# Kernel optimization log

Hardware: AMD Instinct MI355X
Metric: run time of the kernel (lower is better)

The kernel has to match this reference:

```python
import jax, jax.numpy as jnp
import numpy as np

N = 100000   # nodes
E = 600000   # edges
F = 128      # node_feat
HID = 128    # hidden
H = 4        # heads
D = HID // H # head dim
NT = 3       # node types
ET = 4       # edge types
SLOPE = 0.2  # leaky relu slope for attention logits


def hetero_linear(x, types, W, b):
    # per-type linear: out[n] = x[n] @ W[types[n]] + b[types[n]]
    # one-hot contraction avoids gathering a full [N,in,out] weight tensor
    T = W.shape[0]
    oh = jax.nn.one_hot(types, T, dtype=x.dtype)
    return jnp.einsum('ni,nt,tio->no', x, oh, W) + b[types]


def setup_inputs() -> dict:
    key = jax.random.key(0)
    ks = jax.random.split(key, 20)
    f32 = jnp.float32
    s_in = 1.0 / np.sqrt(F)
    s_h = 1.0 / np.sqrt(HID)
    inp = {
        'x': jax.random.normal(ks[0], (N, F), f32),
        'edge_index': jax.random.randint(ks[1], (2, E), 0, N),
        'node_type': jax.random.randint(ks[2], (N,), 0, NT),
        'edge_type': jax.random.randint(ks[3], (E,), 0, ET),
        'edge_attr': jax.random.normal(ks[4], (E, 1), f32),
        # EHATConv params: per-node-type q/k/v projections
        'Wq': jax.random.normal(ks[5], (NT, F, HID), f32) * s_in,
        'Wk': jax.random.normal(ks[6], (NT, F, HID), f32) * s_in,
        'Wv': jax.random.normal(ks[7], (NT, F, HID), f32) * s_in,
        # per-head attention vectors
        'att_src': jax.random.normal(ks[8], (H, D), f32) * s_h,
        'att_dst': jax.random.normal(ks[9], (H, D), f32) * s_h,
        'att_edge': jax.random.normal(ks[10], (H, D), f32) * s_h,
        # per-edge-type edge-attr embedding (edge_dim=1 -> hidden)
        'We': jax.random.normal(ks[11], (ET, 1, HID), f32),
        'be': jax.random.normal(ks[12], (ET, HID), f32) * s_h,
        # HeteroLinear classifiers
        'Wn': jax.random.normal(ks[13], (NT, HID, 1), f32) * s_h,
        'bn': jnp.zeros((NT, 1), f32),
        'Wec': jax.random.normal(ks[14], (ET, HID, 1), f32) * s_h,
        'bec': jnp.zeros((ET, 1), f32),
    }
    return inp


def reference(x, edge_index, node_type, edge_type, edge_attr,
              Wq, Wk, Wv, att_src, att_dst, att_edge, We, be, Wn, bn, Wec, bec):
    src, dst = edge_index[0], edge_index[1]
    n = x.shape[0]
    e = edge_type.shape[0]

    # forward passes zeros as edge_attr into the conv (as in original module)
    eattr = jnp.zeros((e, 1), x.dtype)

    # per-node-type q/k/v projections -> [N,H,D]
    q = hetero_linear(x, node_type, Wq, jnp.zeros((NT, HID), x.dtype)).reshape(n, H, D)
    k = hetero_linear(x, node_type, Wk, jnp.zeros((NT, HID), x.dtype)).reshape(n, H, D)
    v = hetero_linear(x, node_type, Wv, jnp.zeros((NT, HID), x.dtype)).reshape(n, H, D)

    # per-edge-type edge-attr embedding -> [E,H,D]
    e_emb = (jnp.einsum('ni,nio->no', eattr, We[edge_type]) + be[edge_type]).reshape(e, H, D)

    # attention logits per edge/head
    logits = (jnp.einsum('ehd,hd->eh', k[src], att_src)
              + jnp.einsum('ehd,hd->eh', q[dst], att_dst)
              + jnp.einsum('ehd,hd->eh', e_emb, att_edge))
    logits = jnp.where(logits >= 0, logits, SLOPE * logits)

    # segment softmax over incoming edges of each destination node
    m = jax.ops.segment_max(logits, dst, num_segments=n)  # [N,H]
    p = jnp.exp(logits - m[dst])
    denom = jax.ops.segment_sum(p, dst, num_segments=n)   # [N,H]
    alpha = p / (denom[dst] + 1e-16)                       # [E,H]

    # messages and aggregation
    msg = (v[src] + e_emb) * alpha[:, :, None]             # [E,H,D]
    e_out = msg.reshape(e, HID)
    x_out = jax.ops.segment_sum(e_out, dst, num_segments=n)  # [N,HID]

    # nonlin (relu; dropout identity in eval)
    x_h = jax.nn.relu(x_out)
    e_h = jax.nn.relu(e_out)

    # hetero classifiers
    x_cls = hetero_linear(x_h, node_type, Wn, bn)   # [N,1]
    e_cls = hetero_linear(e_h, edge_type, Wec, bec) # [E,1]
    return (x_cls, e_cls)
```

## Files before the change

kernel.cpp:

```cpp
#include <hip/hip_runtime.h>
#include <hip/hip_bf16.h>


#define NN 100000
#define NE 600000
#define FD 128
#define HIDD 128
#define NH 4
#define DH 32
#define NT 3
#define NET 4
#define SLOPE 0.2f
#define CAP 32
#define NBLK_EDGE 2344
#define NBLK_PRE  33

typedef short bf16x8 __attribute__((ext_vector_type(8)));
typedef float f32x4 __attribute__((ext_vector_type(4)));

#define OFF_V       0UL
#define OFF_KS      25600000UL
#define OFF_QD      27200000UL
#define OFF_R       28800000UL
#define OFF_COUNTS  35200000UL
#define OFF_EDGES   35600128UL
#define OFF_ETL     61200128UL
#define OFF_WPACK   61200256UL
#define OFF_BEP     61396864UL
#define OFF_WECP    61398912UL
#define OFF_WNP     61400960UL
#define OFF_WKQP    61402496UL

__device__ __forceinline__ unsigned int pack_bf16(float a, float b) {
    __hip_bfloat16 ha = __float2bfloat16(a);
    __hip_bfloat16 hb = __float2bfloat16(b);
    unsigned short ua = *reinterpret_cast<unsigned short*>(&ha);
    unsigned short ub = *reinterpret_cast<unsigned short*>(&hb);
    return (unsigned int)ua | ((unsigned int)ub << 16);
}

union U8 { uint4 u; bf16x8 v; };

__global__ void k_build(const int* __restrict__ ei, const int* __restrict__ etype,
                        int* __restrict__ counts, uint2* __restrict__ edges,
                        const float* __restrict__ Wq, const float* __restrict__ Wk,
                        const float* __restrict__ Wv,
                        const float* __restrict__ att_src, const float* __restrict__ att_dst,
                        const float* __restrict__ be, const float* __restrict__ att_edge,
                        const float* __restrict__ Wec, const float* __restrict__ Wn,
                        float* __restrict__ etl, unsigned int* __restrict__ wpack,
                        float* __restrict__ bep, float* __restrict__ wecp,
                        float* __restrict__ wnp, unsigned int* __restrict__ wkqp) {
    if (blockIdx.x >= NBLK_EDGE) {
        int pgid = (blockIdx.x - NBLK_EDGE) * 256 + threadIdx.x;
        if (pgid < 16) {
            int t = pgid >> 2, h = pgid & 3;
            float s = 0.f;
            for (int d = 0; d < DH; ++d) s += be[t * HIDD + h * DH + d] * att_edge[h * DH + d];
            etl[t * NH + h] = s;
        } else if (pgid >= 64 && pgid < 64 + NT * 8 * 4 * 64) {
            int q = pgid - 64;
            int t = q >> 11;
            int rem = q & 2047;
            int ot = rem >> 8;
            int rem2 = rem & 255;
            int kc = rem2 >> 6;
            int l = rem2 & 63;
            int o = ot * 16 + (l & 15);
            int kb = kc * 32 + (l >> 4) * 8;
            unsigned int w[4];
#pragma unroll
            for (int jj = 0; jj < 4; ++jj) {
                float v0 = Wv[((size_t)t * FD + kb + 2 * jj) * HIDD + o];
                float v1 = Wv[((size_t)t * FD + kb + 2 * jj + 1) * HIDD + o];
                w[jj] = pack_bf16(v0, v1);
            }
            uint4 o4 = {w[0], w[1], w[2], w[3]};
            *reinterpret_cast<uint4*>(wpack + (size_t)q * 4) = o4;
        } else if (pgid >= 6208 && pgid < 7616) {
            int p = pgid - 6208;
            int dp = p & 127;
            int col = dp >> 3, ot = dp & 7;
            int od = ot * 16 + col;
            if (p < 512) {
                int t2 = p >> 7;
                bep[p] = be[t2 * HIDD + od];
            } else if (p < 1024) {
                int t2 = (p - 512) >> 7;
                wecp[p - 512] = Wec[t2 * HIDD + od];
            } else {
                int t = (p - 1024) >> 7;
                wnp[p - 1024] = Wn[t * HIDD + od];
            }
        } else if (pgid >= 7616 && pgid < 7616 + NT * 4 * 64) {
            int q2 = pgid - 7616;
            int t = q2 >> 8;
            int rem = q2 & 255;
            int kc = rem >> 6;
            int l = rem & 63;
            int col = l & 15, kg = l >> 4;
            unsigned int w[4];
#pragma unroll
            for (int jj = 0; jj < 4; ++jj) {
                float v01[2];
#pragma unroll
                for (int sub = 0; sub < 2; ++sub) {
                    int k = kc * 32 + kg * 8 + 2 * jj + sub;
                    float s = 0.f;
                    if (col < 4) {
                        const float* wrow = Wk + ((size_t)t * FD + k) * HIDD + col * DH;
                        const float* arow = att_src + col * DH;
                        for (int d = 0; d < DH; ++d) s += wrow[d] * arow[d];
                    } else if (col < 8) {
                        int h = col - 4;
                        const float* wrow = Wq + ((size_t)t * FD + k) * HIDD + h * DH;
                        const float* arow = att_dst + h * DH;
                        for (int d = 0; d < DH; ++d) s += wrow[d] * arow[d];
                    }
                    v01[sub] = s;
                }
                w[jj] = pack_bf16(v01[0], v01[1]);
            }
            uint4 o4 = {w[0], w[1], w[2], w[3]};
            *reinterpret_cast<uint4*>(wkqp + (size_t)q2 * 4) = o4;
        }
        return;
    }
    int i = blockIdx.x * blockDim.x + threadIdx.x;
    if (i < NE) {
        int dst = ei[NE + i];
        int pos = atomicAdd(&counts[dst], 1);
        if (pos < CAP) {
            uint2 rec;
            rec.x = ((unsigned)ei[i] << 2) | (unsigned)etype[i];
            rec.y = (unsigned)i;
            edges[(size_t)dst * CAP + pos] = rec;
        }
    }
}

__global__ __launch_bounds__(256) void k_node(const float* __restrict__ x,
                                              const unsigned short* __restrict__ wpack,
                                              const unsigned short* __restrict__ wkqp,
                                              const int* __restrict__ ntype,
                                              unsigned short* __restrict__ vb, float* __restrict__ ks4,
                                              float* __restrict__ qd4) {
    int wave = threadIdx.x >> 6, lane = threadIdx.x & 63;
    int base = blockIdx.x * 64 + wave * 16;
    if (base >= NN) return;
    int col = lane & 15, kg = lane >> 4;
    int n = base + col;
    int tcol = (n < NN) ? ntype[n] : -1;
    int an = n < NN ? n : NN - 1;

    const float* xp = x + (size_t)an * FD;
    bf16x8 afrag[4];
#pragma unroll
    for (int kc = 0; kc < 4; ++kc) {
        float4 a4 = *reinterpret_cast<const float4*>(xp + kc * 32 + kg * 8);
        float4 b4 = *reinterpret_cast<const float4*>(xp + kc * 32 + kg * 8 + 4);
        U8 u;
        u.u.x = pack_bf16(a4.x, a4.y);
        u.u.y = pack_bf16(a4.z, a4.w);
        u.u.z = pack_bf16(b4.x, b4.y);
        u.u.w = pack_bf16(b4.z, b4.w);
        afrag[kc] = u.v;
    }

    f32x4 acc[8];
#pragma unroll
    for (int ot = 0; ot < 8; ++ot) { f32x4 z = {0.f, 0.f, 0.f, 0.f}; acc[ot] = z; }
    f32x4 akq = {0.f, 0.f, 0.f, 0.f};

    for (int t = 0; t < NT; ++t) {
        if (__ballot(tcol == t) == 0ull) continue;
        bf16x8 am[4];
#pragma unroll
        for (int kc = 0; kc < 4; ++kc) {
            U8 z; z.u.x = z.u.y = z.u.z = z.u.w = 0u;
            am[kc] = (tcol == t) ? afrag[kc] : z.v;
        }
        const unsigned short* wt = wpack + (size_t)t * 8 * 4 * 64 * 8;
        const unsigned short* wq = wkqp + (size_t)t * 4 * 64 * 8;
#pragma unroll
        for (int kc = 0; kc < 4; ++kc) {
            bf16x8 bq = *reinterpret_cast<const bf16x8*>(wq + ((size_t)kc * 64 + lane) * 8);
            akq = __builtin_amdgcn_mfma_f32_16x16x32_bf16(am[kc], bq, akq, 0, 0, 0);
#pragma unroll
            for (int ot = 0; ot < 8; ++ot) {
                bf16x8 b = *reinterpret_cast<const bf16x8*>(wt + ((size_t)(ot * 4 + kc) * 64 + lane) * 8);
                acc[ot] = __builtin_amdgcn_mfma_f32_16x16x32_bf16(am[kc], b, acc[ot], 0, 0, 0);
            }
        }
    }

    int dn[4];
#pragma unroll
    for (int rg = 0; rg < 4; ++rg) dn[rg] = base + kg * 4 + rg;

    if (col < 8) {
        float* dst = (col < 4) ? ks4 : qd4;
        int h = col & 3;
#pragma unroll
        for (int rg = 0; rg < 4; ++rg)
            if (dn[rg] < NN) dst[(size_t)dn[rg] * NH + h] = akq[rg];
    }

#pragma unroll
    for (int rg = 0; rg < 4; ++rg) {
        if (dn[rg] < NN) {
            uint4 o4;
            o4.x = pack_bf16(acc[0][rg], acc[1][rg]);
            o4.y = pack_bf16(acc[2][rg], acc[3][rg]);
            o4.z = pack_bf16(acc[4][rg], acc[5][rg]);
            o4.w = pack_bf16(acc[6][rg], acc[7][rg]);
            *reinterpret_cast<uint4*>(vb + (size_t)dn[rg] * FD + col * 8) = o4;
        }
    }
}

__global__ __launch_bounds__(256) void k_r(const unsigned int* __restrict__ vb32,
                                           const float* __restrict__ bep, const float* __restrict__ wecp,
                                           float* __restrict__ rtab) {
    int tid = threadIdx.x;
    int n = blockIdx.x * 16 + (tid >> 4);
    if (n >= NN) return;
    int j = tid & 15;
    uint4 raw = *reinterpret_cast<const uint4*>(vb32 + (size_t)n * 64 + j * 4);
    float vv[8];
    vv[0] = __uint_as_float(raw.x << 16); vv[1] = __uint_as_float(raw.x & 0xffff0000u);
    vv[2] = __uint_as_float(raw.y << 16); vv[3] = __uint_as_float(raw.y & 0xffff0000u);
    vv[4] = __uint_as_float(raw.z << 16); vv[5] = __uint_as_float(raw.z & 0xffff0000u);
    vv[6] = __uint_as_float(raw.w << 16); vv[7] = __uint_as_float(raw.w & 0xffff0000u);
    float cur[16];
#pragma unroll
    for (int t2 = 0; t2 < NET; ++t2) {
        float4 b0 = *reinterpret_cast<const float4*>(bep + t2 * HIDD + j * 8);
        float4 b1 = *reinterpret_cast<const float4*>(bep + t2 * HIDD + j * 8 + 4);
        float4 w0 = *reinterpret_cast<const float4*>(wecp + t2 * HIDD + j * 8);
        float4 w1 = *reinterpret_cast<const float4*>(wecp + t2 * HIDD + j * 8 + 4);
        cur[t2 * 4 + 0] = fmaxf(vv[0] + b0.x, 0.f) * w0.x + fmaxf(vv[1] + b0.y, 0.f) * w0.y;
        cur[t2 * 4 + 1] = fmaxf(vv[2] + b0.z, 0.f) * w0.z + fmaxf(vv[3] + b0.w, 0.f) * w0.w;
        cur[t2 * 4 + 2] = fmaxf(vv[4] + b1.x, 0.f) * w1.x + fmaxf(vv[5] + b1.y, 0.f) * w1.y;
        cur[t2 * 4 + 3] = fmaxf(vv[6] + b1.z, 0.f) * w1.z + fmaxf(vv[7] + b1.w, 0.f) * w1.w;
    }
    int cb = j & 1;
    float n8[8];
#pragma unroll
    for (int i = 0; i < 8; ++i) {
        float keep = cb ? cur[2 * i + 1] : cur[2 * i];
        float give = cb ? cur[2 * i] : cur[2 * i + 1];
        n8[i] = keep + __shfl_xor(give, 1, 64);
    }
    cb = (j >> 1) & 1;
    float n4[4];
#pragma unroll
    for (int i = 0; i < 4; ++i) {
        float keep = cb ? n8[2 * i + 1] : n8[2 * i];
        float give = cb ? n8[2 * i] : n8[2 * i + 1];
        n4[i] = keep + __shfl_xor(give, 2, 64);
    }
    cb = (j >> 2) & 1;
    float n2[2];
#pragma unroll
    for (int i = 0; i < 2; ++i) {
        float keep = cb ? n4[2 * i + 1] : n4[2 * i];
        float give = cb ? n4[2 * i] : n4[2 * i + 1];
        n2[i] = keep + __shfl_xor(give, 4, 64);
    }
    cb = (j >> 3) & 1;
    float keep = cb ? n2[1] : n2[0];
    float give = cb ? n2[0] : n2[1];
    float tot = keep + __shfl_xor(give, 8, 64);
    rtab[(size_t)n * 16 + j] = tot;
}

__global__ __launch_bounds__(256) void k_main(const int* __restrict__ counts, const uint2* __restrict__ edges,
                                              const float* __restrict__ ks4, const float* __restrict__ qd4,
                                              const float* __restrict__ etl, const unsigned int* __restrict__ vb,
                                              const float* __restrict__ bep, const float* __restrict__ rtab,
                                              const float* __restrict__ bec, const float* __restrict__ wnp,
                                              const float* __restrict__ bn, const int* __restrict__ ntype,
                                              float* __restrict__ out_x, float* __restrict__ out_e) {
    int wave = threadIdx.x >> 6;
    int lane = threadIdx.x & 63;
    int n = blockIdx.x * 4 + wave;
    if (n >= NN) return;
    int dg = counts[n];
    dg = dg < CAP ? dg : CAP;
    int deg = __builtin_amdgcn_readfirstlane(dg);
    size_t rs = (size_t)n * CAP;
    int hh = lane & 3;
    int k0 = lane >> 2;

    float q = qd4[(size_t)n * NH + hh];

    bool act0 = k0 < deg;
    uint2 ed0 = {0u, 0u};
    if (act0) ed0 = edges[rs + k0];
    int s0r = (int)(ed0.x >> 2), et0 = (int)(ed0.x & 3u);
    float e0 = 0.f, rt0 = 0.f;
    if (act0) {
        rt0 = rtab[((size_t)s0r * NET + et0) * NH + hh];
        float l = ks4[(size_t)s0r * NH + hh] + q + etl[et0 * NH + hh];
        l = l >= 0.f ? l : SLOPE * l;
        e0 = __expf(l);
    }
    float dn = e0;
    if (deg > 16) {
        for (int bb = 16; bb < deg; bb += 16) {
            int kk = bb + k0;
            if (kk < deg) {
                uint2 ed = edges[rs + kk];
                int s = (int)(ed.x >> 2), et = (int)(ed.x & 3u);
                float l = ks4[(size_t)s * NH + hh] + q + etl[et * NH + hh];
                l = l >= 0.f ? l : SLOPE * l;
                dn += __expf(l);
            }
        }
    }
#pragma unroll
    for (int off = 4; off < 64; off <<= 1) dn += __shfl_xor(dn, off, 64);
    float inv = 1.0f / (dn + 1e-16f);

    if (act0) {
        float term = e0 * inv * rt0;
        term += __shfl_xor(term, 1, 64);
        term += __shfl_xor(term, 2, 64);
        if (hh == 0) out_e[ed0.y] = term + bec[et0];
    }
    if (deg > 16) {
        for (int bb = 16; bb < deg; bb += 16) {
            int kk = bb + k0;
            if (kk < deg) {
                uint2 ed = edges[rs + kk];
                int s = (int)(ed.x >> 2), et = (int)(ed.x & 3u);
                float l = ks4[(size_t)s * NH + hh] + q + etl[et * NH + hh];
                l = l >= 0.f ? l : SLOPE * l;
                float term = __expf(l) * inv * rtab[((size_t)s * NET + et) * NH + hh];
                term += __shfl_xor(term, 1, 64);
                term += __shfl_xor(term, 2, 64);
                if (hh == 0) out_e[ed.y] = term + bec[et];
            }
        }
    }

    float2 beL0 = *reinterpret_cast<const float2*>(bep + 0 * HIDD + 2 * lane);
    float2 beL1 = *reinterpret_cast<const float2*>(bep + 1 * HIDD + 2 * lane);
    float2 beL2 = *reinterpret_cast<const float2*>(bep + 2 * HIDD + 2 * lane);
    float2 beL3 = *reinterpret_cast<const float2*>(bep + 3 * HIDD + 2 * lane);
    float alpha0 = e0 * inv;
    float ax = 0.f, ay = 0.f;
    int c0 = deg < 16 ? deg : 16;
#define AGGH(J) { \
        uint2 er = edges[rs + (J)]; \
        int sn = (int)(er.x >> 2); int et = (int)(er.x & 3u); \
        unsigned int w = vb[(size_t)sn * 64 + lane]; \
        float a = __shfl(alpha0, 4 * (J) + hh, 64); \
        float2 b2 = et == 0 ? beL0 : et == 1 ? beL1 : et == 2 ? beL2 : beL3; \
        ax = fmaf(a, __uint_as_float(w << 16) + b2.x, ax); \
        ay = fmaf(a, __uint_as_float(w & 0xffff0000u) + b2.y, ay); }
    {
        int j = 0;
        for (; j + 4 <= c0; j += 4) {
            AGGH(j) AGGH(j + 1) AGGH(j + 2) AGGH(j + 3)
        }
        for (; j < c0; ++j) AGGH(j)
    }
#undef AGGH
    if (deg > 16) {
        for (int bb = 16; bb < deg; bb += 16) {
            int kk = bb + k0;
            float al = 0.f;
            if (kk < deg) {
                uint2 ed = edges[rs + kk];
                int s = (int)(ed.x >> 2), et = (int)(ed.x & 3u);
                float l = ks4[(size_t)s * NH + hh] + q + etl[et * NH + hh];
                l = l >= 0.f ? l : SLOPE * l;
                al = __expf(l) * inv;
            }
            int cnt = deg - bb; if (cnt > 16) cnt = 16;
#define AGGH2(J) { \
            uint2 er = edges[rs + bb + (J)]; \
            int sn = (int)(er.x >> 2); int et = (int)(er.x & 3u); \
            unsigned int w = vb[(size_t)sn * 64 + lane]; \
            float a = __shfl(al, 4 * (J) + hh, 64); \
            float2 b2 = et == 0 ? beL0 : et == 1 ? beL1 : et == 2 ? beL2 : beL3; \
            ax = fmaf(a, __uint_as_float(w << 16) + b2.x, ax); \
            ay = fmaf(a, __uint_as_float(w & 0xffff0000u) + b2.y, ay); }
            int j = 0;
            for (; j + 4 <= cnt; j += 4) {
                AGGH2(j) AGGH2(j + 1) AGGH2(j + 2) AGGH2(j + 3)
            }
            for (; j < cnt; ++j) AGGH2(j)
#undef AGGH2
        }
    }

    int t = ntype[n];
    float2 w2 = *reinterpret_cast<const float2*>(wnp + t * HIDD + 2 * lane);
    float s = fmaxf(ax, 0.f) * w2.x + fmaxf(ay, 0.f) * w2.y;
#pragma unroll
    for (int off = 1; off < 64; off <<= 1) s += __shfl_xor(s, off, 64);
    if (lane == 0) out_x[n] = s + bn[t];
}

extern "C" void kernel_launch(void* const* d_in, const int* in_sizes, int n_in,
                              void* d_out, int out_size, void* d_ws, size_t ws_size,
                              hipStream_t stream) {
    const float* x        = (const float*)d_in[0];
    const int*   ei       = (const int*)d_in[1];
    const int*   ntype    = (const int*)d_in[2];
    const int*   etype    = (const int*)d_in[3];
    const float* Wq       = (const float*)d_in[5];
    const float* Wk       = (const float*)d_in[6];
    const float* Wv       = (const float*)d_in[7];
    const float* att_src  = (const float*)d_in[8];
    const float* att_dst  = (const float*)d_in[9];
    const float* att_edge = (const float*)d_in[10];
    const float* be       = (const float*)d_in[12];
    const float* Wn       = (const float*)d_in[13];
    const float* bn       = (const float*)d_in[14];
    const float* Wec      = (const float*)d_in[15];
    const float* bec      = (const float*)d_in[16];

    char* ws = (char*)d_ws;
    unsigned int*   vb32 = (unsigned int*)(ws + OFF_V);
    unsigned short* vb16 = (unsigned short*)(ws + OFF_V);
    float* ks4     = (float*)(ws + OFF_KS);
    float* qd4     = (float*)(ws + OFF_QD);
    float* rtab    = (float*)(ws + OFF_R);
    int*   counts  = (int*)(ws + OFF_COUNTS);
    uint2* edges   = (uint2*)(ws + OFF_EDGES);
    float* etl     = (float*)(ws + OFF_ETL);
    unsigned int* wpack = (unsigned int*)(ws + OFF_WPACK);
    float* bep     = (float*)(ws + OFF_BEP);
    float* wecp    = (float*)(ws + OFF_WECP);
    float* wnp     = (float*)(ws + OFF_WNP);
    unsigned int* wkqp = (unsigned int*)(ws + OFF_WKQP);

    float* out_x = (float*)d_out;
    float* out_e = (float*)d_out + NN;

    hipMemsetAsync(ws + OFF_COUNTS, 0, 400000, stream);
    k_build<<<NBLK_EDGE + NBLK_PRE, 256, 0, stream>>>(ei, etype, counts, edges,
                                                      Wq, Wk, Wv, att_src, att_dst, be, att_edge,
                                                      Wec, Wn, etl, wpack, bep, wecp, wnp, wkqp);
    k_node<<<(NN + 63) / 64, 256, 0, stream>>>(x, (const unsigned short*)wpack,
                                               (const unsigned short*)wkqp, ntype,
                                               vb16, ks4, qd4);
    k_r<<<(NN + 15) / 16, 256, 0, stream>>>(vb32, bep, wecp, rtab);
    k_main<<<(NN + 3) / 4, 256, 0, stream>>>(counts, edges, ks4, qd4, etl, vb32, bep,
                                             rtab, bec, wnp, bn, ntype, out_x, out_e);
}
```

Before: 180.2 us.

## Merge edge bucketing into node projection kernel and fold count reset into prep

The memset of the per-destination counts is folded into a small weight-prep kernel, which now runs alone first. The edge-bucketing atomics move from the prep kernel into the node-projection kernel as extra blocks. The goal is to drop one launch plus the memset and let the bandwidth-heavy node GEMM overlap with the atomic scatter of edges. In exchange, the 33-block prep kernel now sits on the critical path by itself, and the mixed kernel's block scheduling may be uneven.

```diff
diff --git a/kernel.cpp b/kernel.cpp
--- a/kernel.cpp
+++ b/kernel.cpp
@@ -12,6 +12,7 @@
 #define NET 4
 #define SLOPE 0.2f
 #define CAP 32
+#define NBLK_NODE 1563
 #define NBLK_EDGE 2344
 #define NBLK_PRE  33
 
@@ -41,110 +42,113 @@
 
 union U8 { uint4 u; bf16x8 v; };
 
-__global__ void k_build(const int* __restrict__ ei, const int* __restrict__ etype,
-                        int* __restrict__ counts, uint2* __restrict__ edges,
-                        const float* __restrict__ Wq, const float* __restrict__ Wk,
-                        const float* __restrict__ Wv,
-                        const float* __restrict__ att_src, const float* __restrict__ att_dst,
-                        const float* __restrict__ be, const float* __restrict__ att_edge,
-                        const float* __restrict__ Wec, const float* __restrict__ Wn,
-                        float* __restrict__ etl, unsigned int* __restrict__ wpack,
-                        float* __restrict__ bep, float* __restrict__ wecp,
-                        float* __restrict__ wnp, unsigned int* __restrict__ wkqp) {
-    if (blockIdx.x >= NBLK_EDGE) {
-        int pgid = (blockIdx.x - NBLK_EDGE) * 256 + threadIdx.x;
-        if (pgid < 16) {
-            int t = pgid >> 2, h = pgid & 3;
-            float s = 0.f;
-            for (int d = 0; d < DH; ++d) s += be[t * HIDD + h * DH + d] * att_edge[h * DH + d];
-            etl[t * NH + h] = s;
-        } else if (pgid >= 64 && pgid < 64 + NT * 8 * 4 * 64) {
-            int q = pgid - 64;
-            int t = q >> 11;
-            int rem = q & 2047;
-            int ot = rem >> 8;
-            int rem2 = rem & 255;
-            int kc = rem2 >> 6;
-            int l = rem2 & 63;
-            int o = ot * 16 + (l & 15);
-            int kb = kc * 32 + (l >> 4) * 8;
-            unsigned int w[4];
-#pragma unroll
-            for (int jj = 0; jj < 4; ++jj) {
-                float v0 = Wv[((size_t)t * FD + kb + 2 * jj) * HIDD + o];
-                float v1 = Wv[((size_t)t * FD + kb + 2 * jj + 1) * HIDD + o];
-                w[jj] = pack_bf16(v0, v1);
-            }
-            uint4 o4 = {w[0], w[1], w[2], w[3]};
-            *reinterpret_cast<uint4*>(wpack + (size_t)q * 4) = o4;
-        } else if (pgid >= 6208 && pgid < 7616) {
-            int p = pgid - 6208;
-            int dp = p & 127;
-            int col = dp >> 3, ot = dp & 7;
-            int od = ot * 16 + col;
-            if (p < 512) {
-                int t2 = p >> 7;
-                bep[p] = be[t2 * HIDD + od];
-            } else if (p < 1024) {
-                int t2 = (p - 512) >> 7;
-                wecp[p - 512] = Wec[t2 * HIDD + od];
-            } else {
-                int t = (p - 1024) >> 7;
-                wnp[p - 1024] = Wn[t * HIDD + od];
-            }
-        } else if (pgid >= 7616 && pgid < 7616 + NT * 4 * 64) {
-            int q2 = pgid - 7616;
-            int t = q2 >> 8;
-            int rem = q2 & 255;
-            int kc = rem >> 6;
-            int l = rem & 63;
-            int col = l & 15, kg = l >> 4;
-            unsigned int w[4];
-#pragma unroll
-            for (int jj = 0; jj < 4; ++jj) {
-                float v01[2];
-#pragma unroll
-                for (int sub = 0; sub < 2; ++sub) {
-                    int k = kc * 32 + kg * 8 + 2 * jj + sub;
-                    float s = 0.f;
-                    if (col < 4) {
-                        const float* wrow = Wk + ((size_t)t * FD + k) * HIDD + col * DH;
-                        const float* arow = att_src + col * DH;
-                        for (int d = 0; d < DH; ++d) s += wrow[d] * arow[d];
-                    } else if (col < 8) {
-                        int h = col - 4;
-                        const float* wrow = Wq + ((size_t)t * FD + k) * HIDD + h * DH;
-                        const float* arow = att_dst + h * DH;
-                        for (int d = 0; d < DH; ++d) s += wrow[d] * arow[d];
-                    }
-                    v01[sub] = s;
+__global__ void k_pre(const float* __restrict__ Wq, const float* __restrict__ Wk,
+                      const float* __restrict__ Wv,
+                      const float* __restrict__ att_src, const float* __restrict__ att_dst,
+                      const float* __restrict__ be, const float* __restrict__ att_edge,
+                      const float* __restrict__ Wec, const float* __restrict__ Wn,
+                      int* __restrict__ counts,
+                      float* __restrict__ etl, unsigned int* __restrict__ wpack,
+                      float* __restrict__ bep, float* __restrict__ wecp,
+                      float* __restrict__ wnp, unsigned int* __restrict__ wkqp) {
+    int pgid = blockIdx.x * 256 + threadIdx.x;
+    for (int i = pgid; i < NN; i += NBLK_PRE * 256) counts[i] = 0;
+    if (pgid < 16) {
+        int t = pgid >> 2, h = pgid & 3;
+        float s = 0.f;
+        for (int d = 0; d < DH; ++d) s += be[t * HIDD + h * DH + d] * att_edge[h * DH + d];
+        etl[t * NH + h] = s;
+    } else if (pgid >= 64 && pgid < 64 + NT * 8 * 4 * 64) {
+        int q = pgid - 64;
+        int t = q >> 11;
+        int rem = q & 2047;
+        int ot = rem >> 8;
+        int rem2 = rem & 255;
+        int kc = rem2 >> 6;
+        int l = rem2 & 63;
+        int o = ot * 16 + (l & 15);
+        int kb = kc * 32 + (l >> 4) * 8;
+        unsigned int w[4];
+#pragma unroll
+        for (int jj = 0; jj < 4; ++jj) {
+            float v0 = Wv[((size_t)t * FD + kb + 2 * jj) * HIDD + o];
+            float v1 = Wv[((size_t)t * FD + kb + 2 * jj + 1) * HIDD + o];
+            w[jj] = pack_bf16(v0, v1);
+        }
+        uint4 o4 = {w[0], w[1], w[2], w[3]};
+        *reinterpret_cast<uint4*>(wpack + (size_t)q * 4) = o4;
+    } else if (pgid >= 6208 && pgid < 7616) {
+        int p = pgid - 6208;
+        int dp = p & 127;
+        int col = dp >> 3, ot = dp & 7;
+        int od = ot * 16 + col;
+        if (p < 512) {
+            int t2 = p >> 7;
+            bep[p] = be[t2 * HIDD + od];
+        } else if (p < 1024) {
+            int t2 = (p - 512) >> 7;
+            wecp[p - 512] = Wec[t2 * HIDD + od];
+        } else {
+            int t = (p - 1024) >> 7;
+            wnp[p - 1024] = Wn[t * HIDD + od];
+        }
+    } else if (pgid >= 7616 && pgid < 7616 + NT * 4 * 64) {
+        int q2 = pgid - 7616;
+        int t = q2 >> 8;
+        int rem = q2 & 255;
+        int kc = rem >> 6;
+        int l = rem & 63;
+        int col = l & 15, kg = l >> 4;
+        unsigned int w[4];
+#pragma unroll
+        for (int jj = 0; jj < 4; ++jj) {
+            float v01[2];
+#pragma unroll
+            for (int sub = 0; sub < 2; ++sub) {
+                int k = kc * 32 + kg * 8 + 2 * jj + sub;
+                float s = 0.f;
+                if (col < 4) {
+                    const float* wrow = Wk + ((size_t)t * FD + k) * HIDD + col * DH;
+                    const float* arow = att_src + col * DH;
+                    for (int d = 0; d < DH; ++d) s += wrow[d] * arow[d];
+                } else if (col < 8) {
+                    int h = col - 4;
+                    const float* wrow = Wq + ((size_t)t * FD + k) * HIDD + h * DH;
+                    const float* arow = att_dst + h * DH;
+                    for (int d = 0; d < DH; ++d) s += wrow[d] * arow[d];
                 }
-                w[jj] = pack_bf16(v01[0], v01[1]);
-            }
-            uint4 o4 = {w[0], w[1], w[2], w[3]};
-            *reinterpret_cast<uint4*>(wkqp + (size_t)q2 * 4) = o4;
-        }
-        return;
-    }
-    int i = blockIdx.x * blockDim.x + threadIdx.x;
-    if (i < NE) {
-        int dst = ei[NE + i];
-        int pos = atomicAdd(&counts[dst], 1);
-        if (pos < CAP) {
-            uint2 rec;
-            rec.x = ((unsigned)ei[i] << 2) | (unsigned)etype[i];
-            rec.y = (unsigned)i;
-            edges[(size_t)dst * CAP + pos] = rec;
-        }
-    }
-}
-
-__global__ __launch_bounds__(256) void k_node(const float* __restrict__ x,
+                v01[sub] = s;
+            }
+            w[jj] = pack_bf16(v01[0], v01[1]);
+        }
+        uint4 o4 = {w[0], w[1], w[2], w[3]};
+        *reinterpret_cast<uint4*>(wkqp + (size_t)q2 * 4) = o4;
+    }
+}
+
+__global__ __launch_bounds__(256) void k_work(const float* __restrict__ x,
                                               const unsigned short* __restrict__ wpack,
                                               const unsigned short* __restrict__ wkqp,
                                               const int* __restrict__ ntype,
                                               unsigned short* __restrict__ vb, float* __restrict__ ks4,
-                                              float* __restrict__ qd4) {
+                                              float* __restrict__ qd4,
+                                              const int* __restrict__ ei, const int* __restrict__ etype,
+                                              int* __restrict__ counts, uint2* __restrict__ edges) {
+    if (blockIdx.x >= NBLK_NODE) {
+        int i = (blockIdx.x - NBLK_NODE) * 256 + threadIdx.x;
+        if (i < NE) {
+            int dst = ei[NE + i];
+            int pos = atomicAdd(&counts[dst], 1);
+            if (pos < CAP) {
+                uint2 rec;
+                rec.x = ((unsigned)ei[i] << 2) | (unsigned)etype[i];
+                rec.y = (unsigned)i;
+                edges[(size_t)dst * CAP + pos] = rec;
+            }
+        }
+        return;
+    }
+
     int wave = threadIdx.x >> 6, lane = threadIdx.x & 63;
     int base = blockIdx.x * 64 + wave * 16;
     if (base >= NN) return;
@@ -442,13 +446,12 @@
     float* out_x = (float*)d_out;
     float* out_e = (float*)d_out + NN;
 
-    hipMemsetAsync(ws + OFF_COUNTS, 0, 400000, stream);
-    k_build<<<NBLK_EDGE + NBLK_PRE, 256, 0, stream>>>(ei, etype, counts, edges,
-                                                      Wq, Wk, Wv, att_src, att_dst, be, att_edge,
-                                                      Wec, Wn, etl, wpack, bep, wecp, wnp, wkqp);
-    k_node<<<(NN + 63) / 64, 256, 0, stream>>>(x, (const unsigned short*)wpack,
-                                               (const unsigned short*)wkqp, ntype,
-                                               vb16, ks4, qd4);
+    k_pre<<<NBLK_PRE, 256, 0, stream>>>(Wq, Wk, Wv, att_src, att_dst, be, att_edge, Wec, Wn,
+                                        counts, etl, wpack, bep, wecp, wnp, wkqp);
+    k_work<<<NBLK_NODE + NBLK_EDGE, 256, 0, stream>>>(x, (const unsigned short*)wpack,
+                                                      (const unsigned short*)wkqp, ntype,
+                                                      vb16, ks4, qd4,
+                                                      ei, etype, counts, edges);
     k_r<<<(NN + 15) / 16, 256, 0, stream>>>(vb32, bep, wecp, rtab);
     k_main<<<(NN + 3) / 4, 256, 0, stream>>>(counts, edges, ks4, qd4, etl, vb32, bep,
                                              rtab, bec, wnp, bn, ntype, out_x, out_e);
```

Result: no change. 179.1 us (-0.6%).
